# Performance work log

Hardware: AMD Instinct MI355X
Metric: run time of the kernel (lower is better)

The kernel has to match this reference:

```python
import jax, jax.numpy as jnp
import numpy as np

# SOLO decoupled-head postprocessing config (TrainConfig)
GRIDS = (40, 36, 24, 16, 12)
STRIDES = (4.0, 8.0, 16.0, 32.0, 64.0)
NMS_PRE = 500
SCORE_THR = 0.1
MASK_THR = 0.005
UPDATE_THR = 0.001
SIGMA = 2.0
MAX_PER_IMG = 100
NUM_CLASSES = 80


def _cell_meta():
    """Per-flattened-cell metadata across the 5 FPN levels (static)."""
    trans_diff, seg_diff, num_grids, strides = [], [], [], []
    t, s = 0, 0
    for g, st in zip(GRIDS, STRIDES):
        n = g * g
        trans_diff.append(np.full(n, t, np.int32))
        seg_diff.append(np.full(n, s, np.int32))
        num_grids.append(np.full(n, g, np.int32))
        strides.append(np.full(n, st, np.float32))
        t += n
        s += g
    return (jnp.asarray(np.concatenate(trans_diff)),
            jnp.asarray(np.concatenate(seg_diff)),
            jnp.asarray(np.concatenate(num_grids)),
            jnp.asarray(np.concatenate(strides)))


def setup_inputs() -> dict:
    key = jax.random.key(0)
    k1, k2, k3 = jax.random.split(key, 3)
    n_cells = sum(g * g for g in GRIDS)   # 3872
    n_rows = sum(GRIDS)                   # 128
    H, W = 200, 304                        # stride-4 map of an 800x1216 image
    return {
        "cate_preds": jax.random.uniform(k1, (n_cells, NUM_CLASSES), jnp.float32),
        "seg_preds_x": jax.random.uniform(k2, (n_rows, H, W), jnp.float32),
        "seg_preds_y": jax.random.uniform(k3, (n_rows, H, W), jnp.float32),
        "ori_h": 427,
        "ori_w": 640,
    }


def _matrix_nms(hardf, labels, scores, sum_masks):
    """Matrix NMS with gaussian decay. hardf: [n, h, w] float, descending scores."""
    n = hardf.shape[0]
    flat = hardf.reshape(n, -1)                      # [n, h*w]
    inter = flat @ flat.T                            # [n, n] pairwise intersection
    union = sum_masks[None, :] + sum_masks[:, None] - inter
    iou = jnp.where(union > 0, inter / jnp.maximum(union, 1e-12), 0.0)
    tri = jnp.triu(jnp.ones((n, n), jnp.float32), 1)  # cols > rows (strict upper)
    same = (labels[None, :] == labels[:, None]) & (labels[:, None] >= 0)
    decay_iou = iou * tri * same.astype(jnp.float32)  # [n, n]
    comp = decay_iou.max(axis=0)                      # max IoU with higher-scored same-class
    decay_m = jnp.exp(-SIGMA * decay_iou ** 2)
    comp_m = jnp.exp(-SIGMA * comp[:, None] ** 2)     # compensate[i, j] = f(comp[i])
    coeff = (decay_m / comp_m).min(axis=0)            # [n]
    return scores * coeff


def reference(cate_preds, seg_preds_x, seg_preds_y, ori_h, ori_w):
    trans_diff, seg_diff, num_grids, strides = _cell_meta()
    C = cate_preds.shape[1]
    flat = cate_preds.reshape(-1)
    flat = jnp.where(flat > SCORE_THR, flat, -1.0)
    scores, idx = jax.lax.top_k(flat, NMS_PRE)        # fixed-size candidate set
    loc = idx // C
    labels = (idx % C).astype(jnp.int32)
    valid = scores > SCORE_THR

    td, sd = trans_diff[loc], seg_diff[loc]
    ng, st = num_grids[loc], strides[loc]
    y_inds = (loc - td) // ng + sd
    x_inds = (loc - td) % ng + sd

    soft = seg_preds_x[x_inds] * seg_preds_y[y_inds]  # [N, H, W]
    hard = soft > MASK_THR
    sum_masks = hard.sum(axis=(1, 2)).astype(jnp.float32)
    keep = valid & (sum_masks > st)
    seg_score = (soft * hard).sum(axis=(1, 2)) / jnp.maximum(sum_masks, 1e-6)
    scores = jnp.where(keep, scores * seg_score, 0.0)
    keepf = keep.astype(jnp.float32)
    hardf = hard.astype(jnp.float32) * keepf[:, None, None]
    sum_masks = sum_masks * keepf
    labels = jnp.where(keep, labels, -1)

    # descending sort (matrix NMS assumes descending scores)
    order = jnp.argsort(-scores)
    scores, labels = scores[order], labels[order]
    soft, hardf, sum_masks = soft[order], hardf[order], sum_masks[order]

    scores = _matrix_nms(hardf, labels, scores, sum_masks)
    scores = jnp.where(scores > UPDATE_THR, scores, 0.0)

    top_scores, top_idx = jax.lax.top_k(scores, MAX_PER_IMG)
    top_soft = soft[top_idx]                          # [100, H, W]
    top_labels = labels[top_idx]

    H, W = top_soft.shape[1], top_soft.shape[2]
    up = jax.image.resize(top_soft, (MAX_PER_IMG, H * 4, W * 4), method="bilinear")
    up = jax.image.resize(up, (MAX_PER_IMG, ori_h, ori_w), method="bilinear")
    seg_masks = (up > MASK_THR).astype(jnp.float32)
    return seg_masks, top_labels, top_scores
```

## Files before the change

kernel.cpp:

```cpp
#include <hip/hip_runtime.h>
#include <stdint.h>

typedef unsigned int u32;
typedef unsigned long long u64;

#define NCELLS  3872
#define NCLS    80
#define NFLAT   309760
#define NPRE    500
#define NPAD    512
#define HH      200
#define WW      304
#define NPIX    60800
#define NWORDS  950
#define MSTRIDE 960
#define MAXOUT  100
#define OH      427
#define OW      640
#define MH      800
#define MW      1216
#define MAXG    4096
#define MAXPAIRS 16384
#define OUT_LBL 27328000
#define OUT_SCR 27328100
#define ROWS_PER_BLK 2
#define NRBLK 214

#define S_THR 0.1f
#define M_THR 0.005f
#define U_THR 0.001f

#define OFF_HIST1   0u
#define OFF_META    263168u
#define ZERO_BYTES  263232u
#define OFF_CAND    263424u
#define OFF_RAW     296192u
#define OFF_LOC     298240u
#define OFF_LABEL   300288u
#define OFF_XIND    302336u
#define OFF_YIND    304384u
#define OFF_STRIDE  306432u
#define OFF_SMF     308480u
#define OFF_SCORE   310528u
#define OFF_LABELK  312576u
#define OFF_ORDER   314624u
#define OFF_SSCORE  316672u
#define OFF_TOPC    318720u
#define OFF_PAIRI   319232u
#define OFF_PAIRIOU 384768u
#define OFF_W1YT0   450304u
#define OFF_W1YA    453504u
#define OFF_W1YB    456704u
#define OFF_W1XT0   459904u
#define OFF_W1XA    464768u
#define OFF_W1XB    469632u
#define OFF_W2YS    474496u
#define OFF_W2YW    476224u
#define OFF_W2XS    483072u
#define OFF_W2XW    485632u
#define OFF_MASKS   495872u
#define OFF_MASKT   4335872u
#define OFF_PARTD   8227072u
#define WS_NEED     12118272u

#define P_U32(off) ((u32*)(ws + (off)))
#define P_I32(off) ((int*)(ws + (off)))
#define P_F32(off) ((float*)(ws + (off)))
#define P_U64(off) ((u64*)(ws + (off)))

__device__ __forceinline__ void levelMeta(int loc, int& td, int& sd, int& ng, float& st) {
  if (loc < 1600)      { td = 0;    sd = 0;   ng = 40; st = 4.f;  }
  else if (loc < 2896) { td = 1600; sd = 40;  ng = 36; st = 8.f;  }
  else if (loc < 3472) { td = 2896; sd = 76;  ng = 24; st = 16.f; }
  else if (loc < 3728) { td = 3472; sd = 100; ng = 16; st = 32.f; }
  else                 { td = 3728; sd = 116; ng = 12; st = 64.f; }
}

__device__ __forceinline__ u32 vbin(float v) {
  int b = (int)(v * 65536.0f);
  if (b > 65535) b = 65535;
  if (b < 0) b = 0;
  return (u32)b;
}

__global__ void kh1(const float* __restrict__ cate, char* __restrict__ ws) {
  int i = blockIdx.x * 256 + threadIdx.x;
  if (i >= NFLAT) return;
  float v = cate[i];
  if (v > S_THR) atomicAdd(&P_U32(OFF_HIST1)[vbin(v)], 1u);
}

__global__ __launch_bounds__(1024) void kc1(char* __restrict__ ws) {
  __shared__ u32 cs[1024];
  __shared__ u32 sfx[1024];
  __shared__ int cbS;
  __shared__ u32 aboveS;
  int t = threadIdx.x;
  const u32* h = P_U32(OFF_HIST1);
  u32 s = 0;
  for (int b = 0; b < 64; b++) s += h[t * 64 + b];
  cs[t] = s; sfx[t] = s;
  if (t == 0) cbS = -1;
  __syncthreads();
  for (int off = 1; off < 1024; off <<= 1) {
    u32 v = (t + off < 1024) ? sfx[t + off] : 0u;
    __syncthreads();
    sfx[t] += v;
    __syncthreads();
  }
  u32 nxt = (t < 1023) ? sfx[t + 1] : 0u;
  if (sfx[t] >= NPRE && nxt < NPRE) { cbS = t; aboveS = nxt; }
  __syncthreads();
  u32* meta = P_U32(OFF_META);
  if (cbS < 0) {
    if (t == 0) { meta[0] = 0u; meta[1] = sfx[0]; meta[2] = 0u; }
    return;
  }
  int cb = cbS;
  if (t < 64) cs[t] = h[cb * 64 + t];
  __syncthreads();
  if (t == 0) {
    u32 cum = aboveS;
    u32 bin = (u32)(cb * 64);
    for (int b = 63; b >= 0; b--) {
      u32 hb = cs[b];
      if (cum + hb >= NPRE) { bin = (u32)(cb * 64 + b); break; }
      cum += hb;
    }
    meta[0] = bin; meta[1] = cum; meta[2] = bin;
  }
}

__global__ void kg(const float* __restrict__ cate, char* __restrict__ ws) {
  u32 key = P_U32(OFF_META)[2];
  int i = blockIdx.x * 256 + threadIdx.x;
  if (i >= NFLAT) return;
  float v = cate[i];
  if (v > S_THR) {
    if (vbin(v) >= key) {
      u32 pos = atomicAdd(&P_U32(OFF_META)[3], 1u);
      if (pos < MAXG) P_U64(OFF_CAND)[pos] = (((u64)__float_as_uint(v)) << 32) | (u32)(~(u32)i);
    }
  }
}

__global__ __launch_bounds__(1024) void kselw(char* __restrict__ ws) {
  __shared__ u64 sk[MAXG];
  int tid = threadIdx.x;
  int G = (int)P_U32(OFF_META)[3]; if (G > MAXG) G = MAXG;
  int n = NPAD;
  while (n < G) n <<= 1;
  const u64* cand = P_U64(OFF_CAND);
  for (int i = tid; i < n; i += 1024) sk[i] = (i < G) ? cand[i] : 0ull;
  __syncthreads();
  for (int k = 2; k <= n; k <<= 1) {
    for (int j = k >> 1; j > 0; j >>= 1) {
      for (int i = tid; i < n; i += 1024) {
        int l = i ^ j;
        if (l > i) {
          u64 a = sk[i], b = sk[l];
          bool sw = ((i & k) == 0) ? (a < b) : (a > b);
          if (sw) { sk[i] = b; sk[l] = a; }
        }
      }
      __syncthreads();
    }
  }
  if (tid < NPAD) {
    float rawv = -1.f; int loc = 0, lab = -1, xi = 0, yi = 0; float st = 3.0e38f;
    if (tid < NPRE && tid < G) {
      u64 key = sk[tid];
      u32 b = (u32)(key >> 32);
      u32 idx = ~((u32)(key & 0xffffffffu));
      rawv = __uint_as_float(b);
      loc = (int)(idx / (u32)NCLS);
      lab = (int)(idx - (u32)loc * NCLS);
      int td, sd, ng; levelMeta(loc, td, sd, ng, st);
      int rel = loc - td;
      int row = rel / ng;
      yi = row + sd;
      xi = (rel - row * ng) + sd;
    }
    P_F32(OFF_RAW)[tid] = rawv;
    P_I32(OFF_LABEL)[tid] = lab;
    P_I32(OFF_XIND)[tid] = xi;
    P_I32(OFF_YIND)[tid] = yi;
    P_F32(OFF_STRIDE)[tid] = st;
    P_F32(OFF_SCORE)[tid] = 0.f;
    P_I32(OFF_LABELK)[tid] = -1;
    P_F32(OFF_SMF)[tid] = 0.f;
  }
  int t = tid;
  for (int r = t; r < MH; r += 1024) {
    float s1 = ((float)r + 0.5f) * 0.25f - 0.5f;
    int t0 = (int)floorf(s1);
    float f = s1 - (float)t0;
    float wa = 1.f - f, wb = f;
    bool ia = (t0 >= 0) && (t0 < HH);
    bool ib = ((t0 + 1) >= 0) && ((t0 + 1) < HH);
    float tw = (ia ? wa : 0.f) + (ib ? wb : 0.f);
    float na = ia ? (wa / tw) : 0.f;
    float nb = ib ? (wb / tw) : 0.f;
    int base; float A, B;
    if (t0 < 0) { base = 0; A = nb; B = 0.f; }
    else if (t0 >= HH - 1) { base = HH - 2; A = 0.f; B = na; }
    else { base = t0; A = na; B = nb; }
    P_I32(OFF_W1YT0)[r] = base;
    P_F32(OFF_W1YA)[r] = A;
    P_F32(OFF_W1YB)[r] = B;
  }
  for (int c = t; c < MW; c += 1024) {
    float s1 = ((float)c + 0.5f) * 0.25f - 0.5f;
    int t0 = (int)floorf(s1);
    float f = s1 - (float)t0;
    float wa = 1.f - f, wb = f;
    bool ia = (t0 >= 0) && (t0 < WW);
    bool ib = ((t0 + 1) >= 0) && ((t0 + 1) < WW);
    float tw = (ia ? wa : 0.f) + (ib ? wb : 0.f);
    float na = ia ? (wa / tw) : 0.f;
    float nb = ib ? (wb / tw) : 0.f;
    int base; float A, B;
    if (t0 < 0) { base = 0; A = nb; B = 0.f; }
    else if (t0 >= WW - 1) { base = WW - 2; A = 0.f; B = na; }
    else { base = t0; A = na; B = nb; }
    P_I32(OFF_W1XT0)[c] = base;
    P_F32(OFF_W1XA)[c] = A;
    P_F32(OFF_W1XB)[c] = B;
  }
  for (int o = t; o < OH; o += 1024) {
    const float inv = (float)(800.0 / 427.0);
    float s2 = ((float)o + 0.5f) * inv - 0.5f;
    int rA = (int)ceilf(s2 - inv);
    int rB = (int)floorf(s2 + inv);
    if (rA < 0) rA = 0;
    if (rB > MH - 1) rB = MH - 1;
    float tot = 0.f;
    for (int r = rA; r <= rB; r++) {
      float x = fabsf(s2 - (float)r) / inv;
      float w = 1.f - x; if (w < 0.f) w = 0.f;
      tot += w;
    }
    int base = rA; if (base > MH - 4) base = MH - 4;
    float o4[4] = {0.f, 0.f, 0.f, 0.f};
    for (int r = rA; r <= rB; r++) {
      float x = fabsf(s2 - (float)r) / inv;
      float w = 1.f - x; if (w < 0.f) w = 0.f;
      o4[r - base] += w / tot;
    }
    P_I32(OFF_W2YS)[o] = base;
    float* wp = P_F32(OFF_W2YW) + o * 4;
    wp[0] = o4[0]; wp[1] = o4[1]; wp[2] = o4[2]; wp[3] = o4[3];
  }
  for (int o = t; o < OW; o += 1024) {
    const float inv = (float)(1216.0 / 640.0);
    float s2 = ((float)o + 0.5f) * inv - 0.5f;
    int rA = (int)ceilf(s2 - inv);
    int rB = (int)floorf(s2 + inv);
    if (rA < 0) rA = 0;
    if (rB > MW - 1) rB = MW - 1;
    float tot = 0.f;
    for (int r = rA; r <= rB; r++) {
      float x = fabsf(s2 - (float)r) / inv;
      float w = 1.f - x; if (w < 0.f) w = 0.f;
      tot += w;
    }
    int base = rA; if (base > MW - 4) base = MW - 4;
    float o4[4] = {0.f, 0.f, 0.f, 0.f};
    for (int r = rA; r <= rB; r++) {
      float x = fabsf(s2 - (float)r) / inv;
      float w = 1.f - x; if (w < 0.f) w = 0.f;
      o4[r - base] += w / tot;
    }
    P_I32(OFF_W2XS)[o] = base;
    float* wp = P_F32(OFF_W2XW) + o * 4;
    wp[0] = o4[0]; wp[1] = o4[1]; wp[2] = o4[2]; wp[3] = o4[3];
  }
}

__global__ __launch_bounds__(256) void kmaskA(const float* __restrict__ segx, const float* __restrict__ segy,
                                              char* __restrict__ ws) {
  __shared__ float lx[128 * 64];
  __shared__ float ly[128 * 64];
  int w0 = blockIdx.x;
  int base = w0 << 6;
  int tid = threadIdx.x;
  for (int idx = tid; idx < 128 * 64; idx += 256) {
    int r = idx >> 6, col = idx & 63;
    int sw = col ^ (r & 63);
    lx[(r << 6) + sw] = segx[(size_t)r * NPIX + base + col];
    ly[(r << 6) + sw] = segy[(size_t)r * NPIX + base + col];
  }
  __syncthreads();
  const int* xind = P_I32(OFF_XIND);
  const int* yind = P_I32(OFF_YIND);
  u64* maskT = P_U64(OFF_MASKT) + (size_t)w0 * NPAD;
  double* partD = (double*)(ws + OFF_PARTD) + (size_t)w0 * NPAD;
  for (int c = tid; c < NPRE; c += 256) {
    int xi = xind[c], yi = yind[c];
    const float* rx = &lx[xi << 6];
    const float* ry = &ly[yi << 6];
    int xk = xi & 63, yk = yi & 63;
    u32 lo = 0, hi = 0;
    double sum = 0.0;
    #pragma unroll 8
    for (int p = 0; p < 32; p++) {
      float s = rx[p ^ xk] * ry[p ^ yk];
      if (s > M_THR) { lo |= (1u << p); sum += (double)s; }
    }
    #pragma unroll 8
    for (int p = 32; p < 64; p++) {
      float s = rx[p ^ xk] * ry[p ^ yk];
      if (s > M_THR) { hi |= (1u << (p - 32)); sum += (double)s; }
    }
    maskT[c] = (((u64)hi) << 32) | lo;
    partD[c] = sum;
  }
}

__global__ __launch_bounds__(256) void kmaskB(char* __restrict__ ws) {
  __shared__ double cd[256];
  __shared__ int ci[256];
  int c = blockIdx.x;
  int tid = threadIdx.x;
  const u64* maskT = P_U64(OFF_MASKT);
  const double* partD = (const double*)(ws + OFF_PARTD);
  double ds = 0.0; int cnt = 0;
  for (int w = tid; w < NWORDS; w += 256) {
    ds += partD[(size_t)w * NPAD + c];
    cnt += (int)__popcll(maskT[(size_t)w * NPAD + c]);
  }
  cd[tid] = ds; ci[tid] = cnt;
  __syncthreads();
  for (int s2 = 128; s2 > 0; s2 >>= 1) {
    if (tid < s2) { ci[tid] += ci[tid + s2]; cd[tid] += cd[tid + s2]; }
    __syncthreads();
  }
  if (tid == 0) {
    float sm = (float)ci[0];
    float rawv = P_F32(OFF_RAW)[c];
    bool valid = rawv > S_THR;
    bool keep = valid && (sm > P_F32(OFF_STRIDE)[c]);
    float ssf = (float)cd[0];
    float segsc = ssf / fmaxf(sm, 1e-6f);
    P_F32(OFF_SCORE)[c] = keep ? (rawv * segsc) : 0.f;
    P_F32(OFF_SMF)[c] = keep ? sm : 0.f;
    P_I32(OFF_LABELK)[c] = keep ? P_I32(OFF_LABEL)[c] : -1;
  }
}

__global__ __launch_bounds__(256) void ktrans(char* __restrict__ ws) {
  __shared__ u64 tile[64][65];
  int w0 = blockIdx.x << 6;
  int c0 = blockIdx.y << 6;
  int tid = threadIdx.x;
  const u64* maskT = P_U64(OFF_MASKT);
  for (int idx = tid; idx < 64 * 64; idx += 256) {
    int rw = idx >> 6, cc = idx & 63;
    int w = w0 + rw;
    tile[rw][cc] = (w < NWORDS) ? maskT[(size_t)w * NPAD + (c0 + cc)] : 0ull;
  }
  __syncthreads();
  u64* masks = P_U64(OFF_MASKS);
  for (int idx = tid; idx < 64 * 64; idx += 256) {
    int rc = idx >> 6, wwi = idx & 63;
    int c = c0 + rc, w = w0 + wwi;
    if (c < NPRE && w < NWORDS) masks[(size_t)c * MSTRIDE + w] = tile[wwi][rc];
  }
}

__global__ __launch_bounds__(256) void kmask(const float* __restrict__ segx, const float* __restrict__ segy,
                                             char* __restrict__ ws) {
  int c = blockIdx.x;
  int tid = threadIdx.x;
  int lane = tid & 63, wv = tid >> 6;
  const float* X = segx + (size_t)P_I32(OFF_XIND)[c] * NPIX;
  const float* Y = segy + (size_t)P_I32(OFF_YIND)[c] * NPIX;
  u64* mrow = P_U64(OFF_MASKS) + (size_t)c * MSTRIDE;
  int cnt = 0;
  double ssum = 0.0;
  for (int w0 = wv; w0 < NWORDS; w0 += 4) {
    int p = (w0 << 6) + lane;
    float s = X[p] * Y[p];
    bool b = s > M_THR;
    u64 bal = __ballot(b ? 1 : 0);
    if (lane == 0) mrow[w0] = bal;
    if (b) { cnt++; ssum += (double)s; }
  }
  __shared__ int ci[256];
  __shared__ double cd[256];
  ci[tid] = cnt; cd[tid] = ssum;
  __syncthreads();
  for (int s2 = 128; s2 > 0; s2 >>= 1) {
    if (tid < s2) { ci[tid] += ci[tid + s2]; cd[tid] += cd[tid + s2]; }
    __syncthreads();
  }
  if (tid == 0) {
    float sm = (float)ci[0];
    float rawv = P_F32(OFF_RAW)[c];
    bool valid = rawv > S_THR;
    bool keep = valid && (sm > P_F32(OFF_STRIDE)[c]);
    float ssf = (float)cd[0];
    float segsc = ssf / fmaxf(sm, 1e-6f);
    P_F32(OFF_SCORE)[c] = keep ? (rawv * segsc) : 0.f;
    P_F32(OFF_SMF)[c] = keep ? sm : 0.f;
    P_I32(OFF_LABELK)[c] = keep ? P_I32(OFF_LABEL)[c] : -1;
  }
}

__global__ __launch_bounds__(512) void ksp(char* __restrict__ ws) {
  __shared__ u64 sk[NPAD];
  __shared__ short slab[NPAD];
  __shared__ u32 scan[NPAD];
  int t = threadIdx.x;
  float sc = (t < NPRE) ? P_F32(OFF_SCORE)[t] : 0.f;
  sk[t] = (((u64)__float_as_uint(sc)) << 32) | (u32)(NPAD - 1 - t);
  __syncthreads();
  for (int k = 2; k <= NPAD; k <<= 1) {
    for (int j = k >> 1; j > 0; j >>= 1) {
      int l = t ^ j;
      if (l > t) {
        u64 a = sk[t], b = sk[l];
        bool sw = ((t & k) == 0) ? (a < b) : (a > b);
        if (sw) { sk[t] = b; sk[l] = a; }
      }
      __syncthreads();
    }
  }
  int ord = NPAD - 1 - (int)(sk[t] & 0xffffffffu);
  P_I32(OFF_ORDER)[t] = ord;
  P_F32(OFF_SSCORE)[t] = __uint_as_float((u32)(sk[t] >> 32));
  const int* labelK = P_I32(OFF_LABELK);
  int lab = (t < NPRE) ? labelK[ord] : -1;
  slab[t] = (short)lab;
  __syncthreads();
  u32 cnt = 0;
  if (lab >= 0) {
    short lj = (short)lab;
    for (int i = 0; i < t; i++) if (slab[i] == lj) cnt++;
  }
  scan[t] = cnt;
  __syncthreads();
  for (int off = 1; off < NPAD; off <<= 1) {
    u32 v = (t >= off) ? scan[t - off] : 0u;
    __syncthreads();
    scan[t] += v;
    __syncthreads();
  }
  if (t == NPAD - 1) {
    u32 tot = scan[t];
    P_U32(OFF_META)[4] = (tot > MAXPAIRS) ? MAXPAIRS : tot;
  }
  if (lab >= 0 && cnt) {
    u32 pos = scan[t] - cnt;
    short lj = (short)lab;
    u32* pairI = P_U32(OFF_PAIRI);
    for (int i = 0; i < t; i++) {
      if (slab[i] == lj) {
        if (pos < MAXPAIRS) pairI[pos] = (((u32)i) << 16) | (u32)t;
        pos++;
      }
    }
  }
}

__global__ __launch_bounds__(64) void kpiou(char* __restrict__ ws) {
  int P = (int)P_U32(OFF_META)[4]; if (P > MAXPAIRS) P = MAXPAIRS;
  const int* order = P_I32(OFF_ORDER);
  const float* smf = P_F32(OFF_SMF);
  const u64* masks = P_U64(OFF_MASKS);
  for (int p = blockIdx.x; p < P; p += gridDim.x) {
    u32 ij = P_U32(OFF_PAIRI)[p];
    int oi = order[ij >> 16];
    int oj = order[ij & 0xffffu];
    const u64* mi = masks + (size_t)oi * MSTRIDE;
    const u64* mj = masks + (size_t)oj * MSTRIDE;
    int inter = 0;
    for (int w = threadIdx.x; w < NWORDS; w += 64)
      inter += (int)__popcll(mi[w] & mj[w]);
    for (int off = 32; off > 0; off >>= 1)
      inter += __shfl_down(inter, off);
    if (threadIdx.x == 0) {
      float fi = (float)inter;
      float uni = (smf[oj] + smf[oi]) - fi;
      float iou = (uni > 0.f) ? (fi / fmaxf(uni, 1e-12f)) : 0.f;
      P_F32(OFF_PAIRIOU)[p] = iou;
    }
  }
}

__global__ __launch_bounds__(512) void knms(char* __restrict__ ws, float* __restrict__ out) {
  __shared__ int compI[NPAD];
  __shared__ int coefI[NPAD];
  __shared__ u64 sk[NPAD];
  int t = threadIdx.x;
  int P = (int)P_U32(OFF_META)[4]; if (P > MAXPAIRS) P = MAXPAIRS;
  const u32* pairI = P_U32(OFF_PAIRI);
  const float* pairIou = P_F32(OFF_PAIRIOU);
  const float* sscore = P_F32(OFF_SSCORE);
  const int* order = P_I32(OFF_ORDER);
  const int* labelK = P_I32(OFF_LABELK);
  int* topc = P_I32(OFF_TOPC);
  compI[t] = 0;
  coefI[t] = __float_as_int(1.0f);
  __syncthreads();
  for (int p = t; p < P; p += 512) {
    int j = (int)(pairI[p] & 0xffffu);
    atomicMax(&compI[j], __float_as_int(pairIou[p]));
  }
  __syncthreads();
  for (int p = t; p < P; p += 512) {
    u32 ij = pairI[p];
    int i = (int)(ij >> 16), j = (int)(ij & 0xffffu);
    float x = pairIou[p];
    float c = __int_as_float(compI[i]);
    float x2 = x * x, c2 = c * c;
    float r = (float)exp(-2.0 * ((double)x2 - (double)c2));
    atomicMin(&coefI[j], __float_as_int(r));
  }
  __syncthreads();
  float ns = 0.f;
  if (t < NPRE) {
    ns = sscore[t] * __int_as_float(coefI[t]);
    ns = (ns > U_THR) ? ns : 0.f;
  }
  sk[t] = (((u64)__float_as_uint(ns)) << 32) | (u32)(NPAD - 1 - t);
  __syncthreads();
  for (int k = 2; k <= NPAD; k <<= 1) {
    for (int j = k >> 1; j > 0; j >>= 1) {
      int l = t ^ j;
      if (l > t) {
        u64 a = sk[t], b = sk[l];
        bool sw = ((t & k) == 0) ? (a < b) : (a > b);
        if (sw) { sk[t] = b; sk[l] = a; }
      }
      __syncthreads();
    }
  }
  if (t < MAXOUT) {
    u64 key = sk[t];
    int pos = NPAD - 1 - (int)(key & 0xffffffffu);
    int cand = order[pos];
    topc[t] = cand;
    out[OUT_LBL + t] = (float)labelK[cand];
    out[OUT_SCR + t] = __uint_as_float((u32)(key >> 32));
  }
}

__global__ __launch_bounds__(256) void kout(const float* __restrict__ segx, const float* __restrict__ segy,
                                            char* __restrict__ ws, float* __restrict__ out) {
  __shared__ float ss[4][WW];
  __shared__ float t1s[6][WW];
  __shared__ float yrs[2][MW];
  int flat = blockIdx.x;
  int w = (flat & 7) * 2675 + (flat >> 3);
  int kk = w / NRBLK;
  int r2 = w - kk * NRBLK;
  int oy0 = r2 * ROWS_PER_BLK;
  int nrow = (oy0 + 1 < OH) ? 2 : 1;
  int tid = threadIdx.x;
  int cand = P_I32(OFF_TOPC)[kk];
  const float* X = segx + (size_t)P_I32(OFF_XIND)[cand] * NPIX;
  const float* Y = segy + (size_t)P_I32(OFF_YIND)[cand] * NPIX;
  const int* w2ys = P_I32(OFF_W2YS);
  int rb = w2ys[oy0];
  const int* w1yT0 = P_I32(OFF_W1YT0);
  int smin = w1yT0[rb];
  for (int q = 0; q < 4; q++) {
    int row = smin + q; if (row > HH - 1) row = HH - 1;
    const float* Xr = X + row * WW;
    const float* Yr = Y + row * WW;
    for (int u = tid; u < WW; u += 256) ss[q][u] = Xr[u] * Yr[u];
  }
  __syncthreads();
  const float* w1yA = P_F32(OFF_W1YA);
  const float* w1yB = P_F32(OFF_W1YB);
  for (int mr = 0; mr < 6; mr++) {
    int r = rb + mr; if (r > MH - 1) r = MH - 1;
    int i0 = w1yT0[r] - smin;
    float A = w1yA[r], B = w1yB[r];
    const float* s0 = &ss[i0][0];
    const float* s1 = &ss[i0 + 1][0];
    for (int u = tid; u < WW; u += 256) t1s[mr][u] = fmaf(B, s1[u], A * s0[u]);
  }
  __syncthreads();
  const int* w1xT0 = P_I32(OFF_W1XT0);
  const float* w1xA = P_F32(OFF_W1XA);
  const float* w1xB = P_F32(OFF_W1XB);
  for (int rr = 0; rr < nrow; rr++) {
    int oy = oy0 + rr;
    int off = w2ys[oy] - rb;
    float4 wy = *(const float4*)(P_F32(OFF_W2YW) + oy * 4);
    const float* r0 = &t1s[off][0];
    const float* r1 = &t1s[off + 1][0];
    const float* r2p = &t1s[off + 2][0];
    const float* r3 = &t1s[off + 3][0];
    for (int cc = tid; cc < MW; cc += 256) {
      int u0 = w1xT0[cc];
      float xa = w1xA[cc], xb = w1xB[cc];
      float up0 = fmaf(xb, r0[u0 + 1], xa * r0[u0]);
      float up1 = fmaf(xb, r1[u0 + 1], xa * r1[u0]);
      float up2 = fmaf(xb, r2p[u0 + 1], xa * r2p[u0]);
      float up3 = fmaf(xb, r3[u0 + 1], xa * r3[u0]);
      float v = wy.x * up0;
      v = fmaf(wy.y, up1, v);
      v = fmaf(wy.z, up2, v);
      v = fmaf(wy.w, up3, v);
      yrs[rr][cc] = v;
    }
  }
  __syncthreads();
  const int* w2xS = P_I32(OFF_W2XS);
  for (int rr = 0; rr < nrow; rr++) {
    int oy = oy0 + rr;
    size_t ob = ((size_t)kk * OH + oy) * OW;
    const float* yr = &yrs[rr][0];
    for (int ox = tid; ox < OW; ox += 256) {
      int cb = w2xS[ox];
      float4 wx = *(const float4*)(P_F32(OFF_W2XW) + ox * 4);
      float acc = wx.x * yr[cb];
      acc = fmaf(wx.y, yr[cb + 1], acc);
      acc = fmaf(wx.z, yr[cb + 2], acc);
      acc = fmaf(wx.w, yr[cb + 3], acc);
      out[ob + ox] = (acc > M_THR) ? 1.0f : 0.0f;
    }
  }
}

extern "C" void kernel_launch(void* const* d_in, const int* in_sizes, int n_in,
                              void* d_out, int out_size, void* d_ws, size_t ws_size,
                              hipStream_t stream) {
  (void)in_sizes; (void)n_in; (void)out_size;
  const float* cate = (const float*)d_in[0];
  const float* segx = (const float*)d_in[1];
  const float* segy = (const float*)d_in[2];
  char* ws = (char*)d_ws;
  float* out = (float*)d_out;
  const bool bigws = (ws_size >= (size_t)WS_NEED);

  hipMemsetAsync(ws, 0, ZERO_BYTES, stream);

  dim3 gFlat((NFLAT + 255) / 256);
  hipLaunchKernelGGL(kh1, gFlat, dim3(256), 0, stream, cate, ws);
  hipLaunchKernelGGL(kc1, dim3(1), dim3(1024), 0, stream, ws);
  hipLaunchKernelGGL(kg, gFlat, dim3(256), 0, stream, cate, ws);
  hipLaunchKernelGGL(kselw, dim3(1), dim3(1024), 0, stream, ws);
  if (bigws) {
    hipLaunchKernelGGL(kmaskA, dim3(NWORDS), dim3(256), 0, stream, segx, segy, ws);
    hipLaunchKernelGGL(kmaskB, dim3(NPRE), dim3(256), 0, stream, ws);
    hipLaunchKernelGGL(ktrans, dim3(15, 8), dim3(256), 0, stream, ws);
  } else {
    hipLaunchKernelGGL(kmask, dim3(NPRE), dim3(256), 0, stream, segx, segy, ws);
  }
  hipLaunchKernelGGL(ksp, dim3(1), dim3(512), 0, stream, ws);
  hipLaunchKernelGGL(kpiou, dim3(2048), dim3(64), 0, stream, ws);
  hipLaunchKernelGGL(knms, dim3(1), dim3(512), 0, stream, ws, out);
  hipLaunchKernelGGL(kout, dim3(MAXOUT * NRBLK), dim3(256), 0, stream, segx, segy, ws, out);
}
```

Before: 273.2 us.

## Vectorize candidate kernels, merge mask stats with transpose, streamline upsample kernel

```diff
diff --git a/kernel.cpp b/kernel.cpp
--- a/kernel.cpp
+++ b/kernel.cpp
@@ -85,9 +85,13 @@
 
 __global__ void kh1(const float* __restrict__ cate, char* __restrict__ ws) {
   int i = blockIdx.x * 256 + threadIdx.x;
-  if (i >= NFLAT) return;
-  float v = cate[i];
-  if (v > S_THR) atomicAdd(&P_U32(OFF_HIST1)[vbin(v)], 1u);
+  if (i >= NFLAT / 4) return;
+  float4 v = ((const float4*)cate)[i];
+  u32* h = P_U32(OFF_HIST1);
+  if (v.x > S_THR) atomicAdd(&h[vbin(v.x)], 1u);
+  if (v.y > S_THR) atomicAdd(&h[vbin(v.y)], 1u);
+  if (v.z > S_THR) atomicAdd(&h[vbin(v.z)], 1u);
+  if (v.w > S_THR) atomicAdd(&h[vbin(v.w)], 1u);
 }
 
 __global__ __launch_bounds__(1024) void kc1(char* __restrict__ ws) {
@@ -134,12 +138,16 @@
 __global__ void kg(const float* __restrict__ cate, char* __restrict__ ws) {
   u32 key = P_U32(OFF_META)[2];
   int i = blockIdx.x * 256 + threadIdx.x;
-  if (i >= NFLAT) return;
-  float v = cate[i];
-  if (v > S_THR) {
-    if (vbin(v) >= key) {
-      u32 pos = atomicAdd(&P_U32(OFF_META)[3], 1u);
-      if (pos < MAXG) P_U64(OFF_CAND)[pos] = (((u64)__float_as_uint(v)) << 32) | (u32)(~(u32)i);
+  if (i >= NFLAT / 4) return;
+  float4 v = ((const float4*)cate)[i];
+  u64* cand = P_U64(OFF_CAND);
+  u32* cntp = &P_U32(OFF_META)[3];
+  #pragma unroll
+  for (int q = 0; q < 4; q++) {
+    float f = (q == 0) ? v.x : (q == 1) ? v.y : (q == 2) ? v.z : v.w;
+    if (f > S_THR && vbin(f) >= key) {
+      u32 pos = atomicAdd(cntp, 1u);
+      if (pos < MAXG) cand[pos] = (((u64)__float_as_uint(f)) << 32) | (u32)(~(u32)(i * 4 + q));
     }
   }
 }
@@ -317,54 +325,55 @@
   }
 }
 
-__global__ __launch_bounds__(256) void kmaskB(char* __restrict__ ws) {
-  __shared__ double cd[256];
-  __shared__ int ci[256];
-  int c = blockIdx.x;
+__global__ __launch_bounds__(256) void kmaskBT(char* __restrict__ ws) {
+  __shared__ u64 tile[64][65];
+  int b = blockIdx.x;
   int tid = threadIdx.x;
-  const u64* maskT = P_U64(OFF_MASKT);
-  const double* partD = (const double*)(ws + OFF_PARTD);
-  double ds = 0.0; int cnt = 0;
-  for (int w = tid; w < NWORDS; w += 256) {
-    ds += partD[(size_t)w * NPAD + c];
-    cnt += (int)__popcll(maskT[(size_t)w * NPAD + c]);
-  }
-  cd[tid] = ds; ci[tid] = cnt;
-  __syncthreads();
-  for (int s2 = 128; s2 > 0; s2 >>= 1) {
-    if (tid < s2) { ci[tid] += ci[tid + s2]; cd[tid] += cd[tid + s2]; }
+  if (b < NPRE) {
+    __shared__ double cd[256];
+    __shared__ int ci[256];
+    int c = b;
+    const u64* maskT = P_U64(OFF_MASKT);
+    const double* partD = (const double*)(ws + OFF_PARTD);
+    double ds = 0.0; int cnt = 0;
+    for (int w = tid; w < NWORDS; w += 256) {
+      ds += partD[(size_t)w * NPAD + c];
+      cnt += (int)__popcll(maskT[(size_t)w * NPAD + c]);
+    }
+    cd[tid] = ds; ci[tid] = cnt;
     __syncthreads();
-  }
-  if (tid == 0) {
-    float sm = (float)ci[0];
-    float rawv = P_F32(OFF_RAW)[c];
-    bool valid = rawv > S_THR;
-    bool keep = valid && (sm > P_F32(OFF_STRIDE)[c]);
-    float ssf = (float)cd[0];
-    float segsc = ssf / fmaxf(sm, 1e-6f);
-    P_F32(OFF_SCORE)[c] = keep ? (rawv * segsc) : 0.f;
-    P_F32(OFF_SMF)[c] = keep ? sm : 0.f;
-    P_I32(OFF_LABELK)[c] = keep ? P_I32(OFF_LABEL)[c] : -1;
-  }
-}
-
-__global__ __launch_bounds__(256) void ktrans(char* __restrict__ ws) {
-  __shared__ u64 tile[64][65];
-  int w0 = blockIdx.x << 6;
-  int c0 = blockIdx.y << 6;
-  int tid = threadIdx.x;
-  const u64* maskT = P_U64(OFF_MASKT);
-  for (int idx = tid; idx < 64 * 64; idx += 256) {
-    int rw = idx >> 6, cc = idx & 63;
-    int w = w0 + rw;
-    tile[rw][cc] = (w < NWORDS) ? maskT[(size_t)w * NPAD + (c0 + cc)] : 0ull;
-  }
-  __syncthreads();
-  u64* masks = P_U64(OFF_MASKS);
-  for (int idx = tid; idx < 64 * 64; idx += 256) {
-    int rc = idx >> 6, wwi = idx & 63;
-    int c = c0 + rc, w = w0 + wwi;
-    if (c < NPRE && w < NWORDS) masks[(size_t)c * MSTRIDE + w] = tile[wwi][rc];
+    for (int s2 = 128; s2 > 0; s2 >>= 1) {
+      if (tid < s2) { ci[tid] += ci[tid + s2]; cd[tid] += cd[tid + s2]; }
+      __syncthreads();
+    }
+    if (tid == 0) {
+      float sm = (float)ci[0];
+      float rawv = P_F32(OFF_RAW)[c];
+      bool valid = rawv > S_THR;
+      bool keep = valid && (sm > P_F32(OFF_STRIDE)[c]);
+      float ssf = (float)cd[0];
+      float segsc = ssf / fmaxf(sm, 1e-6f);
+      P_F32(OFF_SCORE)[c] = keep ? (rawv * segsc) : 0.f;
+      P_F32(OFF_SMF)[c] = keep ? sm : 0.f;
+      P_I32(OFF_LABELK)[c] = keep ? P_I32(OFF_LABEL)[c] : -1;
+    }
+  } else {
+    int q = b - NPRE;
+    int w0 = (q % 15) << 6;
+    int c0 = (q / 15) << 6;
+    const u64* maskT = P_U64(OFF_MASKT);
+    for (int idx = tid; idx < 64 * 64; idx += 256) {
+      int rw = idx >> 6, cc = idx & 63;
+      int w = w0 + rw;
+      tile[rw][cc] = (w < NWORDS) ? maskT[(size_t)w * NPAD + (c0 + cc)] : 0ull;
+    }
+    __syncthreads();
+    u64* masks = P_U64(OFF_MASKS);
+    for (int idx = tid; idx < 64 * 64; idx += 256) {
+      int rc = idx >> 6, wwi = idx & 63;
+      int c = c0 + rc, w = w0 + wwi;
+      if (c < NPRE && w < NWORDS) masks[(size_t)c * MSTRIDE + w] = tile[wwi][rc];
+    }
   }
 }
 
@@ -548,7 +557,6 @@
 
 __global__ __launch_bounds__(256) void kout(const float* __restrict__ segx, const float* __restrict__ segy,
                                             char* __restrict__ ws, float* __restrict__ out) {
-  __shared__ float ss[4][WW];
   __shared__ float t1s[6][WW];
   __shared__ float yrs[2][MW];
   int flat = blockIdx.x;
@@ -564,64 +572,74 @@
   const int* w2ys = P_I32(OFF_W2YS);
   int rb = w2ys[oy0];
   const int* w1yT0 = P_I32(OFF_W1YT0);
-  int smin = w1yT0[rb];
-  for (int q = 0; q < 4; q++) {
-    int row = smin + q; if (row > HH - 1) row = HH - 1;
-    const float* Xr = X + row * WW;
-    const float* Yr = Y + row * WW;
-    for (int u = tid; u < WW; u += 256) ss[q][u] = Xr[u] * Yr[u];
-  }
-  __syncthreads();
   const float* w1yA = P_F32(OFF_W1YA);
   const float* w1yB = P_F32(OFF_W1YB);
   for (int mr = 0; mr < 6; mr++) {
     int r = rb + mr; if (r > MH - 1) r = MH - 1;
-    int i0 = w1yT0[r] - smin;
+    int t0 = w1yT0[r];
     float A = w1yA[r], B = w1yB[r];
-    const float* s0 = &ss[i0][0];
-    const float* s1 = &ss[i0 + 1][0];
-    for (int u = tid; u < WW; u += 256) t1s[mr][u] = fmaf(B, s1[u], A * s0[u]);
+    const float* X0 = X + t0 * WW;
+    const float* Y0 = Y + t0 * WW;
+    const float* X1 = X0 + WW;
+    const float* Y1 = Y0 + WW;
+    for (int u = tid; u < WW; u += 256) {
+      float s0 = X0[u] * Y0[u];
+      float s1 = X1[u] * Y1[u];
+      t1s[mr][u] = fmaf(B, s1, A * s0);
+    }
   }
   __syncthreads();
   const int* w1xT0 = P_I32(OFF_W1XT0);
   const float* w1xA = P_F32(OFF_W1XA);
   const float* w1xB = P_F32(OFF_W1XB);
-  for (int rr = 0; rr < nrow; rr++) {
-    int oy = oy0 + rr;
-    int off = w2ys[oy] - rb;
-    float4 wy = *(const float4*)(P_F32(OFF_W2YW) + oy * 4);
-    const float* r0 = &t1s[off][0];
-    const float* r1 = &t1s[off + 1][0];
-    const float* r2p = &t1s[off + 2][0];
-    const float* r3 = &t1s[off + 3][0];
-    for (int cc = tid; cc < MW; cc += 256) {
-      int u0 = w1xT0[cc];
-      float xa = w1xA[cc], xb = w1xB[cc];
-      float up0 = fmaf(xb, r0[u0 + 1], xa * r0[u0]);
-      float up1 = fmaf(xb, r1[u0 + 1], xa * r1[u0]);
-      float up2 = fmaf(xb, r2p[u0 + 1], xa * r2p[u0]);
-      float up3 = fmaf(xb, r3[u0 + 1], xa * r3[u0]);
-      float v = wy.x * up0;
-      v = fmaf(wy.y, up1, v);
-      v = fmaf(wy.z, up2, v);
-      v = fmaf(wy.w, up3, v);
-      yrs[rr][cc] = v;
+  float4 wy0 = *(const float4*)(P_F32(OFF_W2YW) + oy0 * 4);
+  int oy1 = (nrow == 2) ? (oy0 + 1) : oy0;
+  float4 wy1 = *(const float4*)(P_F32(OFF_W2YW) + oy1 * 4);
+  int off1 = w2ys[oy1] - rb;
+  for (int cc = tid; cc < MW; cc += 256) {
+    int u0 = w1xT0[cc];
+    float xa = w1xA[cc], xb = w1xB[cc];
+    float up0 = fmaf(xb, t1s[0][u0 + 1], xa * t1s[0][u0]);
+    float up1 = fmaf(xb, t1s[1][u0 + 1], xa * t1s[1][u0]);
+    float up2 = fmaf(xb, t1s[2][u0 + 1], xa * t1s[2][u0]);
+    float up3 = fmaf(xb, t1s[3][u0 + 1], xa * t1s[3][u0]);
+    float up4 = fmaf(xb, t1s[4][u0 + 1], xa * t1s[4][u0]);
+    float up5 = fmaf(xb, t1s[5][u0 + 1], xa * t1s[5][u0]);
+    float v0 = wy0.x * up0;
+    v0 = fmaf(wy0.y, up1, v0);
+    v0 = fmaf(wy0.z, up2, v0);
+    v0 = fmaf(wy0.w, up3, v0);
+    yrs[0][cc] = v0;
+    if (nrow == 2) {
+      float a, b2, c3, d;
+      if (off1 == 1)      { a = up1; b2 = up2; c3 = up3; d = up4; }
+      else if (off1 == 2) { a = up2; b2 = up3; c3 = up4; d = up5; }
+      else                { a = up0; b2 = up1; c3 = up2; d = up3; }
+      float v1 = wy1.x * a;
+      v1 = fmaf(wy1.y, b2, v1);
+      v1 = fmaf(wy1.z, c3, v1);
+      v1 = fmaf(wy1.w, d, v1);
+      yrs[1][cc] = v1;
     }
   }
   __syncthreads();
   const int* w2xS = P_I32(OFF_W2XS);
-  for (int rr = 0; rr < nrow; rr++) {
-    int oy = oy0 + rr;
-    size_t ob = ((size_t)kk * OH + oy) * OW;
-    const float* yr = &yrs[rr][0];
-    for (int ox = tid; ox < OW; ox += 256) {
-      int cb = w2xS[ox];
-      float4 wx = *(const float4*)(P_F32(OFF_W2XW) + ox * 4);
-      float acc = wx.x * yr[cb];
-      acc = fmaf(wx.y, yr[cb + 1], acc);
-      acc = fmaf(wx.z, yr[cb + 2], acc);
-      acc = fmaf(wx.w, yr[cb + 3], acc);
-      out[ob + ox] = (acc > M_THR) ? 1.0f : 0.0f;
+  size_t ob0 = ((size_t)kk * OH + oy0) * OW;
+  size_t ob1 = ob0 + OW;
+  for (int ox = tid; ox < OW; ox += 256) {
+    int cb = w2xS[ox];
+    float4 wx = *(const float4*)(P_F32(OFF_W2XW) + ox * 4);
+    float a0 = wx.x * yrs[0][cb];
+    a0 = fmaf(wx.y, yrs[0][cb + 1], a0);
+    a0 = fmaf(wx.z, yrs[0][cb + 2], a0);
+    a0 = fmaf(wx.w, yrs[0][cb + 3], a0);
+    out[ob0 + ox] = (a0 > M_THR) ? 1.0f : 0.0f;
+    if (nrow == 2) {
+      float a1 = wx.x * yrs[1][cb];
+      a1 = fmaf(wx.y, yrs[1][cb + 1], a1);
+      a1 = fmaf(wx.z, yrs[1][cb + 2], a1);
+      a1 = fmaf(wx.w, yrs[1][cb + 3], a1);
+      out[ob1 + ox] = (a1 > M_THR) ? 1.0f : 0.0f;
     }
   }
 }
@@ -639,15 +657,14 @@
 
   hipMemsetAsync(ws, 0, ZERO_BYTES, stream);
 
-  dim3 gFlat((NFLAT + 255) / 256);
-  hipLaunchKernelGGL(kh1, gFlat, dim3(256), 0, stream, cate, ws);
+  dim3 gFlat4((NFLAT / 4 + 255) / 256);
+  hipLaunchKernelGGL(kh1, gFlat4, dim3(256), 0, stream, cate, ws);
   hipLaunchKernelGGL(kc1, dim3(1), dim3(1024), 0, stream, ws);
-  hipLaunchKernelGGL(kg, gFlat, dim3(256), 0, stream, cate, ws);
+  hipLaunchKernelGGL(kg, gFlat4, dim3(256), 0, stream, cate, ws);
   hipLaunchKernelGGL(kselw, dim3(1), dim3(1024), 0, stream, ws);
   if (bigws) {
     hipLaunchKernelGGL(kmaskA, dim3(NWORDS), dim3(256), 0, stream, segx, segy, ws);
-    hipLaunchKernelGGL(kmaskB, dim3(NPRE), dim3(256), 0, stream, ws);
-    hipLaunchKernelGGL(ktrans, dim3(15, 8), dim3(256), 0, stream, ws);
+    hipLaunchKernelGGL(kmaskBT, dim3(NPRE + 120), dim3(256), 0, stream, ws);
   } else {
     hipLaunchKernelGGL(kmask, dim3(NPRE), dim3(256), 0, stream, segx, segy, ws);
   }
```

New measurement: 248.7 us. -9.0%, faster.
